# Kernel optimization log

Measured on AMD Instinct MI355X. Metric: run time of the kernel, lower is better.

Reference implementation:

```python
import jax, jax.numpy as jnp
import numpy as np

N_MOLS = 2048       # number of molecules (segments)
BOND_FDIM = 14      # slice last BOND_FDIM columns of f_bonds
DEPTH = 3


def setup_inputs() -> dict:
    key = jax.random.key(0)
    ks = jax.random.split(key, 12)
    n_atoms, n_bonds = 65536, 131072
    atom_fdim, bond_total, hidden, max_nb = 133, 147, 256, 6
    atom_features = jax.random.normal(ks[0], (n_atoms, atom_fdim), jnp.float32)
    f_bonds = jax.random.normal(ks[1], (n_bonds, bond_total), jnp.float32)
    a2a = jax.random.randint(ks[2], (n_atoms, max_nb), 0, n_atoms, jnp.int32)
    a2b = jax.random.randint(ks[3], (n_atoms, max_nb), 0, n_bonds, jnp.int32)
    segment_ids = jnp.sort(jax.random.randint(ks[4], (n_atoms,), 0, N_MOLS, jnp.int32))
    s = 0.05
    Wi = jax.random.normal(ks[5], (atom_fdim, hidden), jnp.float32) * s
    bi = jax.random.normal(ks[6], (hidden,), jnp.float32) * s
    Wh = jax.random.normal(ks[7], (hidden + BOND_FDIM, hidden), jnp.float32) * s
    bh = jax.random.normal(ks[8], (hidden,), jnp.float32) * s
    Wo = jax.random.normal(ks[9], (atom_fdim + hidden, hidden), jnp.float32) * s
    bo = jax.random.normal(ks[10], (hidden,), jnp.float32) * s
    return {"atom_features": atom_features, "f_bonds": f_bonds, "a2a": a2a,
            "a2b": a2b, "segment_ids": segment_ids,
            "Wi": Wi, "bi": bi, "Wh": Wh, "bh": bh, "Wo": Wo, "bo": bo}


def reference(atom_features, f_bonds, a2a, a2b, segment_ids, Wi, bi, Wh, bh, Wo, bo):
    # W_i + ReLU
    inp = atom_features @ Wi + bi                      # [N, H]
    message = jax.nn.relu(inp)
    fb = f_bonds[:, -BOND_FDIM:]                       # slice last bond_fdim cols
    # depth-1 message passing steps
    for _ in range(DEPTH - 1):
        nei_a_sum = message[a2a].sum(axis=1)           # [N, H]   gather + sum
        nei_b_sum = fb[a2b].sum(axis=1)                # [N, Fb]  gather + sum
        # sum(concat) == concat(sums) over neighbor axis
        m = jnp.concatenate([nei_a_sum, nei_b_sum], axis=1) @ Wh + bh
        message = jax.nn.relu(inp + m)                 # dropout: eval mode (identity)
    # final atom readout
    a_message = message[a2a].sum(axis=1)               # [N, H]
    a_input = jnp.concatenate([atom_features, a_message], axis=1)
    atom_hiddens = jax.nn.relu(a_input @ Wo + bo)      # [N, H]
    # segment-mean pooling over molecules (empty segments -> zero vector)
    sums = jax.ops.segment_sum(atom_hiddens, segment_ids, num_segments=N_MOLS)
    counts = jax.ops.segment_sum(jnp.ones((atom_hiddens.shape[0],), atom_hiddens.dtype),
                                 segment_ids, num_segments=N_MOLS)
    vecs = jnp.where(counts[:, None] > 0, sums / jnp.maximum(counts, 1.0)[:, None], 0.0)
    return vecs
```

## Files before the change

### kernel.cpp

```cpp
#include <hip/hip_runtime.h>

#define N_ATOMS 65536
#define AF      133
#define BT      147
#define HID     256
#define NNB     6
#define NM      2048

#define KI   160
#define KB   32
#define KP   256
#define LSI  168
#define LSB  40
#define LSP  264

typedef __attribute__((ext_vector_type(8))) short short8;
typedef __attribute__((ext_vector_type(4))) float f32x4;

__device__ __forceinline__ unsigned short f2bf(float f) {
    unsigned u = __builtin_bit_cast(unsigned, f);
    u += 0x7fffu + ((u >> 16) & 1u);
    return (unsigned short)(u >> 16);
}
__device__ __forceinline__ float bf2f(unsigned short s) {
    unsigned u = ((unsigned)s) << 16;
    return __builtin_bit_cast(float, u);
}

__global__ __launch_bounds__(256) void k_prep_bond(const float* __restrict__ Wi,
                                                   const float* __restrict__ Wh,
                                                   const float* __restrict__ Wo,
                                                   const float* __restrict__ bi,
                                                   const float* __restrict__ bh,
                                                   const float* __restrict__ f_bonds,
                                                   const int* __restrict__ a2b,
                                                   unsigned short* __restrict__ Wi_t,
                                                   unsigned short* __restrict__ Wb_t,
                                                   unsigned short* __restrict__ Whm_t,
                                                   unsigned short* __restrict__ Woa_t,
                                                   unsigned short* __restrict__ Wom_t,
                                                   unsigned short* __restrict__ bondsum,
                                                   float* __restrict__ b_ih) {
    if (blockIdx.x < 256) {
        const int n = blockIdx.x;
        if (n == 0) b_ih[threadIdx.x] = bi[threadIdx.x] + bh[threadIdx.x];
        for (int k = threadIdx.x; k < KI; k += 256) {
            Wi_t[n * KI + k]  = f2bf(k < AF ? Wi[k * HID + n] : 0.f);
            Woa_t[n * KI + k] = f2bf(k < AF ? Wo[k * HID + n] : 0.f);
        }
        for (int k = threadIdx.x; k < KB; k += 256)
            Wb_t[n * KB + k] = f2bf(k < 14 ? Wh[(HID + k) * HID + n] : 0.f);
        for (int k = threadIdx.x; k < KP; k += 256) {
            Whm_t[n * KP + k] = f2bf(Wh[k * HID + n]);
            Wom_t[n * KP + k] = f2bf(Wo[(AF + k) * HID + n]);
        }
    } else {
        const int id   = (blockIdx.x - 256) * 256 + threadIdx.x;
        const int atom = id >> 4;
        const int c    = id & 15;
        float s = 0.f;
        if (c < 14) {
            const int* nb = &a2b[atom * NNB];
#pragma unroll
            for (int t = 0; t < NNB; ++t)
                s += f_bonds[(size_t)nb[t] * BT + (BT - 14) + c];
        }
        bondsum[atom * 32 + c]      = f2bf(s);
        bondsum[atom * 32 + 16 + c] = 0;
    }
}

template<int K, int LS, int RT>
__device__ __forceinline__ void mfma_core(const unsigned short* __restrict__ As,
                                          const unsigned short* __restrict__ Wt,
                                          f32x4 (&acc)[RT][4], int wave, int lane) {
    const int lm = lane & 15, quad = lane >> 4;
    for (int ks = 0; ks < K; ks += 32) {
        short8 af[RT], bf[4];
#pragma unroll
        for (int rt = 0; rt < RT; ++rt)
            af[rt] = *(const short8*)&As[(rt * 16 + lm) * LS + ks + quad * 8];
#pragma unroll
        for (int ct = 0; ct < 4; ++ct)
            bf[ct] = *(const short8*)&Wt[(size_t)(wave * 64 + ct * 16 + lm) * K + ks + quad * 8];
#pragma unroll
        for (int rt = 0; rt < RT; ++rt)
#pragma unroll
            for (int ct = 0; ct < 4; ++ct)
                acc[rt][ct] = __builtin_amdgcn_mfma_f32_16x16x32_bf16(af[rt], bf[ct], acc[rt][ct], 0, 0, 0);
    }
}

__device__ __forceinline__ void epi_to_lds(f32x4 (&acc)[2][4],
                                           const float* __restrict__ bias,
                                           bool relu_,
                                           unsigned short* __restrict__ E,
                                           int wave, int lane) {
    const int lm = lane & 15, quad = lane >> 4;
#pragma unroll
    for (int ct = 0; ct < 4; ++ct) {
        int col = wave * 64 + ct * 16 + lm;
        float bv = bias ? bias[col] : 0.f;
#pragma unroll
        for (int rt = 0; rt < 2; ++rt)
#pragma unroll
            for (int i = 0; i < 4; ++i) {
                float v = acc[rt][ct][i] + bv;
                if (relu_) v = fmaxf(v, 0.f);
                E[(rt * 16 + quad * 4 + i) * LSP + col] = f2bf(v);
            }
    }
}

__device__ __forceinline__ void store_tile32(unsigned short* __restrict__ dst, int base,
                                             const unsigned short* __restrict__ E, int tid) {
#pragma unroll
    for (int k = 0; k < 4; ++k) {
        int j = k * 256 + tid;
        int r = j >> 5, g = j & 31;
        *(short8*)&dst[(size_t)(base + r) * HID + g * 8] = *(const short8*)&E[r * LSP + g * 8];
    }
}

__global__ __launch_bounds__(256, 4) void k_inp(const float* __restrict__ atom,
                                                const unsigned short* __restrict__ bondsum,
                                                const unsigned short* __restrict__ Wi_t,
                                                const unsigned short* __restrict__ Wb_t,
                                                const unsigned short* __restrict__ Whm_t,
                                                const unsigned short* __restrict__ Woa_t,
                                                const float* __restrict__ bi,
                                                const float* __restrict__ b_ih,
                                                const float* __restrict__ bo,
                                                unsigned short* __restrict__ P0,
                                                unsigned short* __restrict__ inp2,
                                                unsigned short* __restrict__ aw) {
    __shared__ unsigned short big[32 * LSP];
    __shared__ unsigned short bs[32 * LSB];
    const int tid  = threadIdx.x;
    const int base = blockIdx.x * 32;

    for (int it = tid; it < 32 * KI; it += 256) {
        int r = it / KI, c = it - r * KI;
        big[r * LSI + c] = f2bf(c < AF ? atom[(size_t)(base + r) * AF + c] : 0.f);
    }
    if (tid < 128) {
        int r = tid >> 2, c = (tid & 3) * 8;
        *(short8*)&bs[r * LSB + c] = *(const short8*)&bondsum[(size_t)(base + r) * 32 + c];
    }
    __syncthreads();

    const int lane = tid & 63, wave = tid >> 6;
    f32x4 acc1[2][4] = {}, acc3[2][4] = {};
    mfma_core<KI, LSI, 2>(big, Wi_t,  acc1, wave, lane);
    mfma_core<KI, LSI, 2>(big, Woa_t, acc3, wave, lane);
    __syncthreads();

    epi_to_lds(acc1, bi, true, big, wave, lane);
    __syncthreads();

    f32x4 acc2[2][4] = {};
    mfma_core<KP, LSP, 2>(big, Whm_t, acc2, wave, lane);
    mfma_core<KB, LSB, 2>(bs,  Wb_t,  acc1, wave, lane);
    __syncthreads();

    epi_to_lds(acc2, nullptr, false, big, wave, lane);
    __syncthreads();
    store_tile32(P0, base, big, tid);
    __syncthreads();
    epi_to_lds(acc1, b_ih, false, big, wave, lane);
    __syncthreads();
    store_tile32(inp2, base, big, tid);
    __syncthreads();
    epi_to_lds(acc3, bo, false, big, wave, lane);
    __syncthreads();
    store_tile32(aw, base, big, tid);
}

__global__ __launch_bounds__(256) void k_it(const unsigned short* __restrict__ Pin,
                                            const unsigned short* __restrict__ base_,
                                            const int* __restrict__ a2a,
                                            const unsigned short* __restrict__ Wt,
                                            unsigned short* __restrict__ Pout) {
    __shared__ unsigned short mT[32 * LSP];
    __shared__ int nb_l[32 * NNB];
    const int tid  = threadIdx.x;
    const int base = blockIdx.x * 32;

    if (tid < 32 * NNB) nb_l[tid] = a2a[base * NNB + tid];
    __syncthreads();

#pragma unroll
    for (int k = 0; k < 4; ++k) {
        int j = k * 256 + tid;
        int r = j >> 5, g = j & 31;
        const int* nb = &nb_l[r * NNB];
        float s[8] = {};
#pragma unroll
        for (int t = 0; t < NNB; ++t) {
            short8 u = *(const short8*)&Pin[(size_t)nb[t] * HID + g * 8];
#pragma unroll
            for (int q = 0; q < 8; ++q) s[q] += bf2f((unsigned short)u[q]);
        }
        short8 b = *(const short8*)&base_[(size_t)(base + r) * HID + g * 8];
        short8 o;
#pragma unroll
        for (int q = 0; q < 8; ++q)
            o[q] = (short)f2bf(fmaxf(s[q] + bf2f((unsigned short)b[q]), 0.f));
        *(short8*)&mT[r * LSP + g * 8] = o;
    }
    __syncthreads();

    const int lane = tid & 63, wave = tid >> 6;
    f32x4 acc[2][4] = {};
    mfma_core<KP, LSP, 2>(mT, Wt, acc, wave, lane);
    __syncthreads();
    epi_to_lds(acc, nullptr, false, mT, wave, lane);
    __syncthreads();
    store_tile32(Pout, base, mT, tid);
}

__global__ __launch_bounds__(256) void k_gseg(const unsigned short* __restrict__ P,
                                              const unsigned short* __restrict__ aw,
                                              const int* __restrict__ a2a,
                                              const int* __restrict__ seg,
                                              float* __restrict__ out) {
    const int m = blockIdx.x;
    __shared__ int lohi[2];
    if (threadIdx.x == 0) {
        int lo = 0, hi = N_ATOMS;
        while (lo < hi) { int mid = (lo + hi) >> 1; if (seg[mid] < m) lo = mid + 1; else hi = mid; }
        lohi[0] = lo;
        int lo2 = lo, hi2 = N_ATOMS;
        while (lo2 < hi2) { int mid = (lo2 + hi2) >> 1; if (seg[mid] < m + 1) lo2 = mid + 1; else hi2 = mid; }
        lohi[1] = lo2;
    }
    __syncthreads();
    const int lo = lohi[0], hi = lohi[1];
    const int j = threadIdx.x;
    float s = 0.f;
#pragma unroll 2
    for (int i = lo; i < hi; ++i) {
        const int* nb = &a2a[i * NNB];
        float v = bf2f(aw[(size_t)i * HID + j]);
#pragma unroll
        for (int t = 0; t < NNB; ++t)
            v += bf2f(P[(size_t)nb[t] * HID + j]);
        s += fmaxf(v, 0.f);
    }
    const int cnt = hi - lo;
    out[m * HID + j] = (cnt > 0) ? (s / (float)cnt) : 0.f;
}

extern "C" void kernel_launch(void* const* d_in, const int* in_sizes, int n_in,
                              void* d_out, int out_size, void* d_ws, size_t ws_size,
                              hipStream_t stream) {
    const float* atom    = (const float*)d_in[0];
    const float* f_bonds = (const float*)d_in[1];
    const int*   a2a     = (const int*)d_in[2];
    const int*   a2b     = (const int*)d_in[3];
    const int*   seg     = (const int*)d_in[4];
    const float* Wi      = (const float*)d_in[5];
    const float* bi      = (const float*)d_in[6];
    const float* Wh      = (const float*)d_in[7];
    const float* bh      = (const float*)d_in[8];
    const float* Wo      = (const float*)d_in[9];
    const float* bo      = (const float*)d_in[10];
    float* out = (float*)d_out;

    unsigned short* ws = (unsigned short*)d_ws;
    const size_t nh = (size_t)N_ATOMS * HID;
    unsigned short* Pa   = ws;
    unsigned short* Pb   = Pa + nh;
    unsigned short* inp2 = Pb + nh;
    unsigned short* aw   = inp2 + nh;
    unsigned short* bsum = aw + nh;
    unsigned short* Wi_t  = bsum + (size_t)N_ATOMS * 32;
    unsigned short* Wb_t  = Wi_t + 256 * KI;
    unsigned short* Whm_t = Wb_t + 256 * KB;
    unsigned short* Woa_t = Whm_t + 256 * KP;
    unsigned short* Wom_t = Woa_t + 256 * KI;
    float*          b_ih  = (float*)(Wom_t + 256 * KP);

    dim3 blk(256);
    const int nb32 = N_ATOMS / 32;

    k_prep_bond<<<256 + N_ATOMS * 16 / 256, blk, 0, stream>>>(
        Wi, Wh, Wo, bi, bh, f_bonds, a2b,
        Wi_t, Wb_t, Whm_t, Woa_t, Wom_t, bsum, b_ih);
    k_inp<<<nb32, blk, 0, stream>>>(atom, bsum, Wi_t, Wb_t, Whm_t, Woa_t,
                                    bi, b_ih, bo, Pa, inp2, aw);

    k_it<<<nb32, blk, 0, stream>>>(Pa, inp2, a2a, Whm_t, Pb);
    k_it<<<nb32, blk, 0, stream>>>(Pb, inp2, a2a, Wom_t, Pa);
    k_gseg<<<NM, blk, 0, stream>>>(Pa, aw, a2a, seg, out);
}
```

Measured before the change: 385.4 us.

## Fuse dual-weight MFMA loop, split LDS buffers, and vectorize segment readout

The input kernel now computes the Wi and Wo-atom products in one MFMA loop that shares the A-fragment loads, and stores the aw tile early from a separate work buffer so the atom tile stays intact. The iteration kernel gets a higher occupancy hint and a non-unrolled gather loop to lower register pressure. The readout kernel is restructured so each thread handles 8 columns with 16-byte loads, 8 atoms are processed in parallel per block, and the partial sums are reduced through shared memory. This is meant to cut redundant LDS reads and the scalar 2-byte gather traffic in the readout. In exchange it uses more LDS and adds a reduction step.

Measured after the change: 375.8 us. 2.5% less time.

```diff
diff --git a/kernel.cpp b/kernel.cpp
--- a/kernel.cpp
+++ b/kernel.cpp
@@ -70,24 +70,52 @@
     }
 }
 
-template<int K, int LS, int RT>
+template<int K, int LS>
 __device__ __forceinline__ void mfma_core(const unsigned short* __restrict__ As,
                                           const unsigned short* __restrict__ Wt,
-                                          f32x4 (&acc)[RT][4], int wave, int lane) {
+                                          f32x4 (&acc)[2][4], int wave, int lane) {
     const int lm = lane & 15, quad = lane >> 4;
     for (int ks = 0; ks < K; ks += 32) {
-        short8 af[RT], bf[4];
-#pragma unroll
-        for (int rt = 0; rt < RT; ++rt)
+        short8 af[2], bf[4];
+#pragma unroll
+        for (int rt = 0; rt < 2; ++rt)
             af[rt] = *(const short8*)&As[(rt * 16 + lm) * LS + ks + quad * 8];
 #pragma unroll
         for (int ct = 0; ct < 4; ++ct)
             bf[ct] = *(const short8*)&Wt[(size_t)(wave * 64 + ct * 16 + lm) * K + ks + quad * 8];
 #pragma unroll
-        for (int rt = 0; rt < RT; ++rt)
+        for (int rt = 0; rt < 2; ++rt)
 #pragma unroll
             for (int ct = 0; ct < 4; ++ct)
                 acc[rt][ct] = __builtin_amdgcn_mfma_f32_16x16x32_bf16(af[rt], bf[ct], acc[rt][ct], 0, 0, 0);
+    }
+}
+
+template<int K, int LS>
+__device__ __forceinline__ void mfma_core2(const unsigned short* __restrict__ As,
+                                           const unsigned short* __restrict__ WtA,
+                                           const unsigned short* __restrict__ WtB,
+                                           f32x4 (&accA)[2][4], f32x4 (&accB)[2][4],
+                                           int wave, int lane) {
+    const int lm = lane & 15, quad = lane >> 4;
+    for (int ks = 0; ks < K; ks += 32) {
+        short8 af[2], bfA[4], bfB[4];
+#pragma unroll
+        for (int rt = 0; rt < 2; ++rt)
+            af[rt] = *(const short8*)&As[(rt * 16 + lm) * LS + ks + quad * 8];
+#pragma unroll
+        for (int ct = 0; ct < 4; ++ct) {
+            size_t off = (size_t)(wave * 64 + ct * 16 + lm) * K + ks + quad * 8;
+            bfA[ct] = *(const short8*)&WtA[off];
+            bfB[ct] = *(const short8*)&WtB[off];
+        }
+#pragma unroll
+        for (int rt = 0; rt < 2; ++rt)
+#pragma unroll
+            for (int ct = 0; ct < 4; ++ct) {
+                accA[rt][ct] = __builtin_amdgcn_mfma_f32_16x16x32_bf16(af[rt], bfA[ct], accA[rt][ct], 0, 0, 0);
+                accB[rt][ct] = __builtin_amdgcn_mfma_f32_16x16x32_bf16(af[rt], bfB[ct], accB[rt][ct], 0, 0, 0);
+            }
     }
 }
 
@@ -134,14 +162,15 @@
                                                 unsigned short* __restrict__ P0,
                                                 unsigned short* __restrict__ inp2,
                                                 unsigned short* __restrict__ aw) {
-    __shared__ unsigned short big[32 * LSP];
+    __shared__ unsigned short atomT[32 * LSI];
+    __shared__ unsigned short work[32 * LSP];
     __shared__ unsigned short bs[32 * LSB];
     const int tid  = threadIdx.x;
     const int base = blockIdx.x * 32;
 
     for (int it = tid; it < 32 * KI; it += 256) {
         int r = it / KI, c = it - r * KI;
-        big[r * LSI + c] = f2bf(c < AF ? atom[(size_t)(base + r) * AF + c] : 0.f);
+        atomT[r * LSI + c] = f2bf(c < AF ? atom[(size_t)(base + r) * AF + c] : 0.f);
     }
     if (tid < 128) {
         int r = tid >> 2, c = (tid & 3) * 8;
@@ -151,36 +180,35 @@
 
     const int lane = tid & 63, wave = tid >> 6;
     f32x4 acc1[2][4] = {}, acc3[2][4] = {};
-    mfma_core<KI, LSI, 2>(big, Wi_t,  acc1, wave, lane);
-    mfma_core<KI, LSI, 2>(big, Woa_t, acc3, wave, lane);
-    __syncthreads();
-
-    epi_to_lds(acc1, bi, true, big, wave, lane);
+    mfma_core2<KI, LSI>(atomT, Wi_t, Woa_t, acc1, acc3, wave, lane);
+
+    epi_to_lds(acc3, bo, false, work, wave, lane);
+    __syncthreads();
+    store_tile32(aw, base, work, tid);
+    __syncthreads();
+
+    epi_to_lds(acc1, bi, true, work, wave, lane);
     __syncthreads();
 
     f32x4 acc2[2][4] = {};
-    mfma_core<KP, LSP, 2>(big, Whm_t, acc2, wave, lane);
-    mfma_core<KB, LSB, 2>(bs,  Wb_t,  acc1, wave, lane);
-    __syncthreads();
-
-    epi_to_lds(acc2, nullptr, false, big, wave, lane);
-    __syncthreads();
-    store_tile32(P0, base, big, tid);
-    __syncthreads();
-    epi_to_lds(acc1, b_ih, false, big, wave, lane);
-    __syncthreads();
-    store_tile32(inp2, base, big, tid);
-    __syncthreads();
-    epi_to_lds(acc3, bo, false, big, wave, lane);
-    __syncthreads();
-    store_tile32(aw, base, big, tid);
-}
-
-__global__ __launch_bounds__(256) void k_it(const unsigned short* __restrict__ Pin,
-                                            const unsigned short* __restrict__ base_,
-                                            const int* __restrict__ a2a,
-                                            const unsigned short* __restrict__ Wt,
-                                            unsigned short* __restrict__ Pout) {
+    mfma_core<KP, LSP>(work, Whm_t, acc2, wave, lane);
+    mfma_core<KB, LSB>(bs, Wb_t, acc1, wave, lane);
+    __syncthreads();
+
+    epi_to_lds(acc2, nullptr, false, work, wave, lane);
+    __syncthreads();
+    store_tile32(P0, base, work, tid);
+    __syncthreads();
+    epi_to_lds(acc1, b_ih, false, work, wave, lane);
+    __syncthreads();
+    store_tile32(inp2, base, work, tid);
+}
+
+__global__ __launch_bounds__(256, 6) void k_it(const unsigned short* __restrict__ Pin,
+                                               const unsigned short* __restrict__ base_,
+                                               const int* __restrict__ a2a,
+                                               const unsigned short* __restrict__ Wt,
+                                               unsigned short* __restrict__ Pout) {
     __shared__ unsigned short mT[32 * LSP];
     __shared__ int nb_l[32 * NNB];
     const int tid  = threadIdx.x;
@@ -189,7 +217,7 @@
     if (tid < 32 * NNB) nb_l[tid] = a2a[base * NNB + tid];
     __syncthreads();
 
-#pragma unroll
+#pragma unroll 1
     for (int k = 0; k < 4; ++k) {
         int j = k * 256 + tid;
         int r = j >> 5, g = j & 31;
@@ -212,20 +240,21 @@
 
     const int lane = tid & 63, wave = tid >> 6;
     f32x4 acc[2][4] = {};
-    mfma_core<KP, LSP, 2>(mT, Wt, acc, wave, lane);
+    mfma_core<KP, LSP>(mT, Wt, acc, wave, lane);
     __syncthreads();
     epi_to_lds(acc, nullptr, false, mT, wave, lane);
     __syncthreads();
     store_tile32(Pout, base, mT, tid);
 }
 
-__global__ __launch_bounds__(256) void k_gseg(const unsigned short* __restrict__ P,
-                                              const unsigned short* __restrict__ aw,
-                                              const int* __restrict__ a2a,
-                                              const int* __restrict__ seg,
-                                              float* __restrict__ out) {
+__global__ __launch_bounds__(256, 6) void k_gseg(const unsigned short* __restrict__ P,
+                                                 const unsigned short* __restrict__ aw,
+                                                 const int* __restrict__ a2a,
+                                                 const int* __restrict__ seg,
+                                                 float* __restrict__ out) {
     const int m = blockIdx.x;
     __shared__ int lohi[2];
+    __shared__ float red[8 * 256];
     if (threadIdx.x == 0) {
         int lo = 0, hi = N_ATOMS;
         while (lo < hi) { int mid = (lo + hi) >> 1; if (seg[mid] < m) lo = mid + 1; else hi = mid; }
@@ -236,19 +265,39 @@
     }
     __syncthreads();
     const int lo = lohi[0], hi = lohi[1];
+    const int slot = threadIdx.x >> 5;
+    const int cg   = threadIdx.x & 31;
+
+    float s[8] = {};
+#pragma unroll 1
+    for (int i0 = lo; i0 < hi; i0 += 8) {
+        int i = i0 + slot;
+        if (i < hi) {
+            const int* nb = &a2a[i * NNB];
+            short8 a = *(const short8*)&aw[(size_t)i * HID + cg * 8];
+            float v[8];
+#pragma unroll
+            for (int q = 0; q < 8; ++q) v[q] = bf2f((unsigned short)a[q]);
+#pragma unroll
+            for (int t = 0; t < NNB; ++t) {
+                short8 u = *(const short8*)&P[(size_t)nb[t] * HID + cg * 8];
+#pragma unroll
+                for (int q = 0; q < 8; ++q) v[q] += bf2f((unsigned short)u[q]);
+            }
+#pragma unroll
+            for (int q = 0; q < 8; ++q) s[q] += fmaxf(v[q], 0.f);
+        }
+    }
+#pragma unroll
+    for (int q = 0; q < 8; ++q) red[slot * 256 + cg * 8 + q] = s[q];
+    __syncthreads();
+
     const int j = threadIdx.x;
-    float s = 0.f;
-#pragma unroll 2
-    for (int i = lo; i < hi; ++i) {
-        const int* nb = &a2a[i * NNB];
-        float v = bf2f(aw[(size_t)i * HID + j]);
-#pragma unroll
-        for (int t = 0; t < NNB; ++t)
-            v += bf2f(P[(size_t)nb[t] * HID + j]);
-        s += fmaxf(v, 0.f);
-    }
+    float tot = 0.f;
+#pragma unroll
+    for (int sl = 0; sl < 8; ++sl) tot += red[sl * 256 + j];
     const int cnt = hi - lo;
-    out[m * HID + j] = (cnt > 0) ? (s / (float)cnt) : 0.f;
+    out[m * HID + j] = (cnt > 0) ? (tot / (float)cnt) : 0.f;
 }
 
 extern "C" void kernel_launch(void* const* d_in, const int* in_sizes, int n_in,
```
